# Optimization experiments

Hardware: AMD Instinct MI355X
Metric: run time of the kernel (lower is better)

Reference implementation:

```python
import jax, jax.numpy as jnp
import numpy as np

NUM_HEADS = 16
EPS = 1e-5
BLOCK = 16  # score_mod: q_idx // 16 == kv_idx % 16


def _ln(x, eps=EPS):
    # LayerNorm, elementwise_affine=False
    m = jnp.mean(x, axis=-1, keepdims=True)
    v = jnp.mean((x - m) ** 2, axis=-1, keepdims=True)
    return (x - m) * jax.lax.rsqrt(v + eps)


def setup_inputs() -> dict:
    key = jax.random.key(0)
    ks = jax.random.split(key, 5)
    N, D = 2048, 2048
    w = 0.02
    return {
        "x": jax.random.normal(ks[0], (N, D), jnp.float32),
        "Wq": jax.random.normal(ks[1], (D, D), jnp.float32) * w,
        "Wk": jax.random.normal(ks[2], (D, D), jnp.float32) * w,
        "Wv": jax.random.normal(ks[3], (D, D), jnp.float32) * w,
        "Wo": jax.random.normal(ks[4], (D, D), jnp.float32) * w,
    }


def reference(x, Wq, Wk, Wv, Wo):
    N, D = x.shape
    H = NUM_HEADS
    DH = D // H
    x_in = x
    xn = _ln(x)
    # per-head q/k layernorm, cast to attention dtype (bfloat16)
    q = _ln((xn @ Wq).reshape(N, H, DH)).astype(jnp.bfloat16)
    k = _ln((xn @ Wk).reshape(N, H, DH)).astype(jnp.bfloat16)
    v = (xn @ Wv).reshape(N, H, DH)  # stays fp32 (original applies no cast to vs)
    scale = 1.0 / np.sqrt(DH)
    # dense scores then sparsity mask, as flex_attention with score_mod does
    scores = jnp.einsum("nhd,mhd->hnm", q, k, preferred_element_type=jnp.float32) * scale
    qi = jnp.arange(N)
    mask = (qi[:, None] // BLOCK) == (qi[None, :] % BLOCK)  # [N, N]
    s = jnp.where(mask[None, :, :], scores, -jnp.inf)
    # safe softmax: rows with no allowed keys (q_idx >= 256) produce zeros
    mx = jnp.max(s, axis=-1, keepdims=True)
    e = jnp.exp(s - jnp.where(jnp.isfinite(mx), mx, 0.0))
    denom = jnp.sum(e, axis=-1, keepdims=True)
    attn = e / jnp.maximum(denom, 1e-30)
    o = jnp.einsum("hnm,mhd->nhd", attn, v)  # [N, H, DH]
    out = o.reshape(N, D) @ Wo
    return out + x_in
```

## Files before the change

kernel.cpp:

```cpp
#include <hip/hip_runtime.h>

typedef unsigned short u16;
typedef __attribute__((ext_vector_type(8))) short short8;
typedef __attribute__((ext_vector_type(4))) float f32x4;

#define D 2048
#define EPS 1e-5f

__device__ __forceinline__ u16 f2bf(float f) {
  unsigned u = __float_as_uint(f);
  u += 0x7fffu + ((u >> 16) & 1u);
  return (u16)(u >> 16);
}

__device__ __forceinline__ void async16(const void* g, void* l) {
  __builtin_amdgcn_global_load_lds(
      (const __attribute__((address_space(1))) void*)g,
      (__attribute__((address_space(3))) void*)l, 16, 0, 0);
}

__global__ __launch_bounds__(256) void prep(const float* __restrict__ x,
                                            const float* __restrict__ Wq,
                                            const float* __restrict__ Wk,
                                            const float* __restrict__ Wv,
                                            const float* __restrict__ Wo,
                                            u16* __restrict__ xn,
                                            float* __restrict__ out,
                                            u16* __restrict__ WqT, u16* __restrict__ WkT,
                                            u16* __restrict__ WvT, u16* __restrict__ WoT) {
  int bid = blockIdx.x;
  int t = threadIdx.x;
  if (bid < 2048) {
    const float* xr = x + (size_t)bid * D;
    float4 v[2];
    float s = 0.f, sq = 0.f;
#pragma unroll
    for (int i = 0; i < 2; i++) {
      v[i] = *(const float4*)(xr + i * 1024 + t * 4);
      s += v[i].x + v[i].y + v[i].z + v[i].w;
      sq += v[i].x * v[i].x + v[i].y * v[i].y + v[i].z * v[i].z + v[i].w * v[i].w;
    }
#pragma unroll
    for (int m = 32; m >= 1; m >>= 1) { s += __shfl_xor(s, m); sq += __shfl_xor(sq, m); }
    __shared__ float ps[4], pq[4];
    int w = t >> 6, lane = t & 63;
    if (lane == 0) { ps[w] = s; pq[w] = sq; }
    __syncthreads();
    s = ps[0] + ps[1] + ps[2] + ps[3];
    sq = pq[0] + pq[1] + pq[2] + pq[3];
    float mean = s * (1.f / D);
    float var = sq * (1.f / D) - mean * mean;
    float rs = rsqrtf(var + EPS);
    float* outr = out + (size_t)bid * D;
    u16* xnr = xn + (size_t)bid * D;
#pragma unroll
    for (int i = 0; i < 2; i++) {
      *(float4*)(outr + i * 1024 + t * 4) = v[i];
      ushort4 o;
      o.x = f2bf((v[i].x - mean) * rs);
      o.y = f2bf((v[i].y - mean) * rs);
      o.z = f2bf((v[i].z - mean) * rs);
      o.w = f2bf((v[i].w - mean) * rs);
      *(ushort4*)(xnr + i * 1024 + t * 4) = o;
    }
  } else {
    int tb = bid - 2048;
    int wsel = tb >> 10;
    int tt = tb & 1023;
    const float* src; u16* dst;
    switch (wsel) {
      case 0: src = Wq; dst = WqT; break;
      case 1: src = Wk; dst = WkT; break;
      case 2: src = Wv; dst = WvT; break;
      default: src = Wo; dst = WoT; break;
    }
    int i0 = (tt >> 5) * 64, j0 = (tt & 31) * 64;
    __shared__ u16 tile[64 * 66];
#pragma unroll
    for (int r = 0; r < 4; r++) {
      int idx = r * 256 + t;
      int row = idx >> 4, c4 = idx & 15;
      float4 v = *(const float4*)(src + (size_t)(i0 + row) * D + j0 + c4 * 4);
      tile[row * 66 + c4 * 4 + 0] = f2bf(v.x);
      tile[row * 66 + c4 * 4 + 1] = f2bf(v.y);
      tile[row * 66 + c4 * 4 + 2] = f2bf(v.z);
      tile[row * 66 + c4 * 4 + 3] = f2bf(v.w);
    }
    __syncthreads();
#pragma unroll
    for (int r = 0; r < 4; r++) {
      int idx = r * 256 + t;
      int row = idx >> 4, c4 = idx & 15;
      ushort4 o;
      o.x = tile[(c4 * 4 + 0) * 66 + row];
      o.y = tile[(c4 * 4 + 1) * 66 + row];
      o.z = tile[(c4 * 4 + 2) * 66 + row];
      o.w = tile[(c4 * 4 + 3) * 66 + row];
      *(ushort4*)(dst + (size_t)(j0 + row) * D + i0 + c4 * 4) = o;
    }
  }
}

__device__ __forceinline__ void gemm_tile(const u16* __restrict__ A,
                                          const u16* __restrict__ Bt,
                                          int m0, int n0,
                                          int kbeg, int kend,
                                          u16* As, u16* Bs, f32x4 acc[4][4]) {
  int tid = threadIdx.x, wid = tid >> 6, lane = tid & 63;
  int q4 = lane >> 4, m16 = lane & 15;
  int wm = wid >> 1, wn = wid & 1;
  for (int kb = kbeg; kb < kend; kb += 64) {
#pragma unroll
    for (int p = 0; p < 4; p++) {
      int idx = p * 256 + tid;
      int r = idx >> 3, sl = idx & 7;
      int gc = sl ^ (r & 7);
      async16(A + (size_t)(m0 + r) * D + kb + gc * 8, As + (size_t)idx * 8);
      async16(Bt + (size_t)(n0 + r) * D + kb + gc * 8, Bs + (size_t)idx * 8);
    }
    __syncthreads();
#pragma unroll
    for (int ks = 0; ks < 2; ks++) {
      short8 af[4], bf[4];
      int c = ks * 4 + q4;
#pragma unroll
      for (int i = 0; i < 4; i++) {
        int ra = wm * 64 + i * 16 + m16;
        af[i] = *(const short8*)(As + ra * 64 + (c ^ (ra & 7)) * 8);
        int rb = wn * 64 + i * 16 + m16;
        bf[i] = *(const short8*)(Bs + rb * 64 + (c ^ (rb & 7)) * 8);
      }
#pragma unroll
      for (int i = 0; i < 4; i++)
#pragma unroll
        for (int j = 0; j < 4; j++)
          acc[i][j] = __builtin_amdgcn_mfma_f32_16x16x32_bf16(af[i], bf[j], acc[i][j], 0, 0, 0);
    }
    __syncthreads();
  }
}

__global__ __launch_bounds__(256, 4) void gemm_mega(const u16* __restrict__ xn,
                                                    const u16* __restrict__ WkT,
                                                    const u16* __restrict__ WqT,
                                                    const u16* __restrict__ WvT,
                                                    u16* __restrict__ K3,
                                                    u16* __restrict__ Q3,
                                                    u16* __restrict__ V3) {
  __shared__ u16 smem[64 * 64 + 128 * 64];
  u16* As = smem;
  u16* Bs = smem + 64 * 64;
  int bid = blockIdx.x;
  int sel = (bid < 512) ? 0 : (bid < 1024) ? 2 : 1;
  int z = (sel == 0) ? bid : (sel == 2) ? bid - 512 : bid - 1024;
  int m0 = (z >> 4) * 64, n0 = (z & 15) * 128;
  const u16* A = (sel == 2) ? WvT : xn;
  const u16* Bt = (sel == 0) ? WkT : (sel == 1) ? WqT : xn;
  bool permB = (sel == 2);

  int tid = threadIdx.x, wid = tid >> 6, lane = tid & 63;
  int q4 = lane >> 4, m16 = lane & 15;
  int wm = wid >> 1, wn = wid & 1;

  f32x4 acc[2][4];
#pragma unroll
  for (int i = 0; i < 2; i++)
#pragma unroll
    for (int j = 0; j < 4; j++)
#pragma unroll
      for (int r = 0; r < 4; r++) acc[i][j][r] = 0.f;

  for (int kb = 0; kb < D; kb += 64) {
#pragma unroll
    for (int p = 0; p < 2; p++) {
      int idx = p * 256 + tid;
      int r = idx >> 3, sl = idx & 7;
      int gc = sl ^ (r & 7);
      async16(A + (size_t)(m0 + r) * D + kb + gc * 8, As + (size_t)idx * 8);
    }
#pragma unroll
    for (int p = 0; p < 4; p++) {
      int idx = p * 256 + tid;
      int r = idx >> 3, sl = idx & 7;
      int gc = sl ^ (r & 7);
      int rb = n0 + r;
      int gr = permB ? ((rb & 127) * 16 + (rb >> 7)) : rb;
      async16(Bt + (size_t)gr * D + kb + gc * 8, Bs + (size_t)idx * 8);
    }
    __syncthreads();
#pragma unroll
    for (int ks = 0; ks < 2; ks++) {
      short8 af[2], bf[4];
      int c = ks * 4 + q4;
#pragma unroll
      for (int i = 0; i < 2; i++) {
        int ra = wm * 32 + i * 16 + m16;
        af[i] = *(const short8*)(As + ra * 64 + (c ^ (ra & 7)) * 8);
      }
#pragma unroll
      for (int j = 0; j < 4; j++) {
        int rb = wn * 64 + j * 16 + m16;
        bf[j] = *(const short8*)(Bs + rb * 64 + (c ^ (rb & 7)) * 8);
      }
#pragma unroll
      for (int i = 0; i < 2; i++)
#pragma unroll
        for (int j = 0; j < 4; j++)
          acc[i][j] = __builtin_amdgcn_mfma_f32_16x16x32_bf16(af[i], bf[j], acc[i][j], 0, 0, 0);
    }
    __syncthreads();
  }

  if (sel == 2) {
    int h = m0 >> 7, b = n0 >> 7;
#pragma unroll
    for (int i = 0; i < 2; i++)
#pragma unroll
      for (int j = 0; j < 4; j++)
#pragma unroll
        for (int r = 0; r < 4; r++) {
          int dhl = (m0 & 127) + wm * 32 + i * 16 + q4 * 4 + r;
          int key = wn * 64 + j * 16 + m16;
          V3[((size_t)(h * 16 + b) * 128 + dhl) * 128 + key] = f2bf(acc[i][j][r]);
        }
  } else {
    float* redS = (float*)smem;
    float* redQ = redS + 128;
    __syncthreads();
#pragma unroll
    for (int i = 0; i < 2; i++) {
      float ps[4], pq[4];
#pragma unroll
      for (int r = 0; r < 4; r++) {
        float s = 0.f, q = 0.f;
#pragma unroll
        for (int j = 0; j < 4; j++) { float a = acc[i][j][r]; s += a; q += a * a; }
#pragma unroll
        for (int msk = 1; msk < 16; msk <<= 1) {
          s += __shfl_xor(s, msk);
          q += __shfl_xor(q, msk);
        }
        ps[r] = s; pq[r] = q;
      }
      if (m16 == 0) {
#pragma unroll
        for (int r = 0; r < 4; r++) {
          int row = wm * 32 + i * 16 + q4 * 4 + r;
          redS[row * 2 + wn] = ps[r];
          redQ[row * 2 + wn] = pq[r];
        }
      }
    }
    __syncthreads();
    int h = n0 >> 7;
#pragma unroll
    for (int i = 0; i < 2; i++)
#pragma unroll
      for (int r = 0; r < 4; r++) {
        int row = wm * 32 + i * 16 + q4 * 4 + r;
        float S = redS[row * 2] + redS[row * 2 + 1];
        float Qs = redQ[row * 2] + redQ[row * 2 + 1];
        float mean = S * (1.f / 128.f);
        float var = Qs * (1.f / 128.f) - mean * mean;
        float rstd = rsqrtf(var + EPS);
        int tok = m0 + row;
#pragma unroll
        for (int j = 0; j < 4; j++) {
          int dhl = wn * 64 + j * 16 + m16;
          u16 val = f2bf((acc[i][j][r] - mean) * rstd);
          if (sel == 0)
            K3[(((size_t)(h * 16 + (tok & 15))) * 128 + (tok >> 4)) * 128 + dhl] = val;
          else
            Q3[((size_t)h * 256 + tok) * 128 + dhl] = val;
        }
      }
  }
}

__global__ __launch_bounds__(128) void attn(const u16* __restrict__ Q3,
                                            const u16* __restrict__ K3,
                                            const u16* __restrict__ V3,
                                            u16* __restrict__ Ob) {
  int bh = blockIdx.x;
  int b = bh & 15, h = bh >> 4;
  int tid = threadIdx.x, w = tid >> 6, lane = tid & 63;
  int q4 = lane >> 4, m16 = lane & 15;
  __shared__ float redmx[2][16];
  __shared__ float redsm[2][16];
  __shared__ float invd[16];
  __shared__ u16 P[16][136];
  const float scale = 0.08838834764831845f;
  const u16* Ktile = K3 + (size_t)(h * 16 + b) * 128 * 128;
  const u16* Vtile = V3 + (size_t)(h * 16 + b) * 128 * 128;

  short8 af[4];
#pragma unroll
  for (int dc = 0; dc < 4; dc++)
    af[dc] = *(const short8*)(Q3 + ((size_t)h * 256 + b * 16 + m16) * 128 + dc * 32 + q4 * 8);
  f32x4 s[4];
#pragma unroll
  for (int kt = 0; kt < 4; kt++)
#pragma unroll
    for (int r = 0; r < 4; r++) s[kt][r] = 0.f;
#pragma unroll
  for (int kt = 0; kt < 4; kt++) {
    int key = w * 64 + kt * 16 + m16;
#pragma unroll
    for (int dc = 0; dc < 4; dc++) {
      short8 bf = *(const short8*)(Ktile + (size_t)key * 128 + dc * 32 + q4 * 8);
      s[kt] = __builtin_amdgcn_mfma_f32_16x16x32_bf16(af[dc], bf, s[kt], 0, 0, 0);
    }
  }
  float mx[4];
#pragma unroll
  for (int r = 0; r < 4; r++) {
    mx[r] = fmaxf(fmaxf(s[0][r], s[1][r]), fmaxf(s[2][r], s[3][r]));
#pragma unroll
    for (int msk = 1; msk < 16; msk <<= 1) mx[r] = fmaxf(mx[r], __shfl_xor(mx[r], msk));
  }
  if (m16 == 0) {
#pragma unroll
    for (int r = 0; r < 4; r++) redmx[w][q4 * 4 + r] = mx[r];
  }
  __syncthreads();
#pragma unroll
  for (int r = 0; r < 4; r++) {
    float M = fmaxf(redmx[0][q4 * 4 + r], redmx[1][q4 * 4 + r]);
    float acc = 0.f;
#pragma unroll
    for (int kt = 0; kt < 4; kt++) {
      float e = __expf((s[kt][r] - M) * scale);
      s[kt][r] = e;
      acc += e;
    }
#pragma unroll
    for (int msk = 1; msk < 16; msk <<= 1) acc += __shfl_xor(acc, msk);
    if (m16 == 0) redsm[w][q4 * 4 + r] = acc;
  }
#pragma unroll
  for (int kt = 0; kt < 4; kt++)
#pragma unroll
    for (int r = 0; r < 4; r++)
      P[q4 * 4 + r][w * 64 + kt * 16 + m16] = f2bf(s[kt][r]);
  __syncthreads();
  if (tid < 16) invd[tid] = 1.0f / (redsm[0][tid] + redsm[1][tid]);
  __syncthreads();

  short8 pf[4];
#pragma unroll
  for (int kc = 0; kc < 4; kc++)
    pf[kc] = *(const short8*)(&P[m16][kc * 32 + q4 * 8]);
  f32x4 o[4];
#pragma unroll
  for (int dt = 0; dt < 4; dt++)
#pragma unroll
    for (int r = 0; r < 4; r++) o[dt][r] = 0.f;
#pragma unroll
  for (int dt = 0; dt < 4; dt++) {
    int dhl = (w * 4 + dt) * 16 + m16;
#pragma unroll
    for (int kc = 0; kc < 4; kc++) {
      short8 vf = *(const short8*)(Vtile + (size_t)dhl * 128 + kc * 32 + q4 * 8);
      o[dt] = __builtin_amdgcn_mfma_f32_16x16x32_bf16(pf[kc], vf, o[dt], 0, 0, 0);
    }
  }
#pragma unroll
  for (int dt = 0; dt < 4; dt++)
#pragma unroll
    for (int r = 0; r < 4; r++) {
      int row = q4 * 4 + r;
      float val = o[dt][r] * invd[row];
      Ob[(size_t)(b * 16 + row) * D + h * 128 + (w * 4 + dt) * 16 + m16] = f2bf(val);
    }
}

__global__ __launch_bounds__(256, 3) void gemm_wo(const u16* __restrict__ Ob,
                                                  const u16* __restrict__ WoT,
                                                  float* __restrict__ Wpart) {
  __shared__ u16 smem[2 * 128 * 64];
  u16* As = smem;
  u16* Bs = smem + 8192;
  int m0 = blockIdx.x * 128, n0 = blockIdx.y * 128;
  int z = blockIdx.z;
  int k0 = z * 256;
  f32x4 acc[4][4];
#pragma unroll
  for (int i = 0; i < 4; i++)
#pragma unroll
    for (int j = 0; j < 4; j++)
#pragma unroll
      for (int r = 0; r < 4; r++) acc[i][j][r] = 0.f;
  gemm_tile(Ob, WoT, m0, n0, k0, k0 + 256, As, Bs, acc);
  float* C = Wpart + (size_t)z * 256 * D;
  int tid = threadIdx.x, wid = tid >> 6, lane = tid & 63;
  int q4 = lane >> 4, m16 = lane & 15;
  int wm = wid >> 1, wn = wid & 1;
#pragma unroll
  for (int i = 0; i < 4; i++)
#pragma unroll
    for (int j = 0; j < 4; j++)
#pragma unroll
      for (int r = 0; r < 4; r++) {
        int row = m0 + wm * 64 + i * 16 + q4 * 4 + r;
        int col = n0 + wn * 64 + j * 16 + m16;
        C[(size_t)row * D + col] = acc[i][j][r];
      }
}

__global__ __launch_bounds__(256) void reduce_wo(const float* __restrict__ Wpart,
                                                 float* __restrict__ out) {
  int i = (blockIdx.x * 256 + threadIdx.x) * 4;
  float4 s = *(const float4*)(out + i);
#pragma unroll
  for (int z = 0; z < 8; z++) {
    float4 p = *(const float4*)(Wpart + (size_t)z * 256 * D + i);
    s.x += p.x; s.y += p.y; s.z += p.z; s.w += p.w;
  }
  *(float4*)(out + i) = s;
}

extern "C" void kernel_launch(void* const* d_in, const int* in_sizes, int n_in,
                              void* d_out, int out_size, void* d_ws, size_t ws_size,
                              hipStream_t stream) {
  const float* x  = (const float*)d_in[0];
  const float* Wq = (const float*)d_in[1];
  const float* Wk = (const float*)d_in[2];
  const float* Wv = (const float*)d_in[3];
  const float* Wo = (const float*)d_in[4];
  float* out = (float*)d_out;
  char* w = (char*)d_ws;
  const size_t MB = 1u << 20;
  u16*   xn    = (u16*)(w);
  u16*   WqT   = (u16*)(w + 8 * MB);
  u16*   WkT   = (u16*)(w + 16 * MB);
  u16*   WvT   = (u16*)(w + 24 * MB);
  u16*   WoT   = (u16*)(w + 32 * MB);
  u16*   K3    = (u16*)(w + 40 * MB);
  u16*   V3    = (u16*)(w + 48 * MB);
  u16*   Q3    = (u16*)(w + 56 * MB);
  u16*   Obf   = (u16*)(w + 57 * MB);
  float* Wpart = (float*)(w + 58 * MB);

  prep<<<dim3(6144), dim3(256), 0, stream>>>(x, Wq, Wk, Wv, Wo, xn, out, WqT, WkT, WvT, WoT);
  gemm_mega<<<dim3(1088), dim3(256), 0, stream>>>(xn, WkT, WqT, WvT, K3, Q3, V3);
  attn<<<dim3(256), dim3(128), 0, stream>>>(Q3, K3, V3, Obf);
  gemm_wo<<<dim3(2, 16, 8), dim3(256), 0, stream>>>(Obf, WoT, Wpart);
  reduce_wo<<<dim3(512), dim3(256), 0, stream>>>(Wpart, out);
}
```

Before: 200.2 us.

## Split prep into layernorm and wide-tile weight transpose, widen attention to four waves

The combined prep kernel is split into a row layernorm kernel and a separate weight transpose-and-convert kernel. The transpose now uses 128x128 tiles and writes 16-byte vectors instead of 8-byte ones, to improve global store coalescing. The attention kernel goes from two to four waves per block, each handling 32 keys and 32 output columns, to spread the small per-block work over more lanes. The trade-off is one extra kernel launch and a larger LDS tile in the transpose kernel.

```diff
diff --git a/kernel.cpp b/kernel.cpp
--- a/kernel.cpp
+++ b/kernel.cpp
@@ -19,85 +19,81 @@
       (__attribute__((address_space(3))) void*)l, 16, 0, 0);
 }
 
-__global__ __launch_bounds__(256) void prep(const float* __restrict__ x,
-                                            const float* __restrict__ Wq,
-                                            const float* __restrict__ Wk,
-                                            const float* __restrict__ Wv,
-                                            const float* __restrict__ Wo,
-                                            u16* __restrict__ xn,
-                                            float* __restrict__ out,
-                                            u16* __restrict__ WqT, u16* __restrict__ WkT,
-                                            u16* __restrict__ WvT, u16* __restrict__ WoT) {
+__global__ __launch_bounds__(256) void ln_rows(const float* __restrict__ x,
+                                               u16* __restrict__ xn,
+                                               float* __restrict__ out) {
   int bid = blockIdx.x;
   int t = threadIdx.x;
-  if (bid < 2048) {
-    const float* xr = x + (size_t)bid * D;
-    float4 v[2];
-    float s = 0.f, sq = 0.f;
-#pragma unroll
-    for (int i = 0; i < 2; i++) {
-      v[i] = *(const float4*)(xr + i * 1024 + t * 4);
-      s += v[i].x + v[i].y + v[i].z + v[i].w;
-      sq += v[i].x * v[i].x + v[i].y * v[i].y + v[i].z * v[i].z + v[i].w * v[i].w;
-    }
-#pragma unroll
-    for (int m = 32; m >= 1; m >>= 1) { s += __shfl_xor(s, m); sq += __shfl_xor(sq, m); }
-    __shared__ float ps[4], pq[4];
-    int w = t >> 6, lane = t & 63;
-    if (lane == 0) { ps[w] = s; pq[w] = sq; }
-    __syncthreads();
-    s = ps[0] + ps[1] + ps[2] + ps[3];
-    sq = pq[0] + pq[1] + pq[2] + pq[3];
-    float mean = s * (1.f / D);
-    float var = sq * (1.f / D) - mean * mean;
-    float rs = rsqrtf(var + EPS);
-    float* outr = out + (size_t)bid * D;
-    u16* xnr = xn + (size_t)bid * D;
-#pragma unroll
-    for (int i = 0; i < 2; i++) {
-      *(float4*)(outr + i * 1024 + t * 4) = v[i];
-      ushort4 o;
-      o.x = f2bf((v[i].x - mean) * rs);
-      o.y = f2bf((v[i].y - mean) * rs);
-      o.z = f2bf((v[i].z - mean) * rs);
-      o.w = f2bf((v[i].w - mean) * rs);
-      *(ushort4*)(xnr + i * 1024 + t * 4) = o;
-    }
-  } else {
-    int tb = bid - 2048;
-    int wsel = tb >> 10;
-    int tt = tb & 1023;
-    const float* src; u16* dst;
-    switch (wsel) {
-      case 0: src = Wq; dst = WqT; break;
-      case 1: src = Wk; dst = WkT; break;
-      case 2: src = Wv; dst = WvT; break;
-      default: src = Wo; dst = WoT; break;
-    }
-    int i0 = (tt >> 5) * 64, j0 = (tt & 31) * 64;
-    __shared__ u16 tile[64 * 66];
-#pragma unroll
-    for (int r = 0; r < 4; r++) {
-      int idx = r * 256 + t;
-      int row = idx >> 4, c4 = idx & 15;
-      float4 v = *(const float4*)(src + (size_t)(i0 + row) * D + j0 + c4 * 4);
-      tile[row * 66 + c4 * 4 + 0] = f2bf(v.x);
-      tile[row * 66 + c4 * 4 + 1] = f2bf(v.y);
-      tile[row * 66 + c4 * 4 + 2] = f2bf(v.z);
-      tile[row * 66 + c4 * 4 + 3] = f2bf(v.w);
-    }
-    __syncthreads();
-#pragma unroll
-    for (int r = 0; r < 4; r++) {
-      int idx = r * 256 + t;
-      int row = idx >> 4, c4 = idx & 15;
-      ushort4 o;
-      o.x = tile[(c4 * 4 + 0) * 66 + row];
-      o.y = tile[(c4 * 4 + 1) * 66 + row];
-      o.z = tile[(c4 * 4 + 2) * 66 + row];
-      o.w = tile[(c4 * 4 + 3) * 66 + row];
-      *(ushort4*)(dst + (size_t)(j0 + row) * D + i0 + c4 * 4) = o;
-    }
+  const float* xr = x + (size_t)bid * D;
+  float4 v[2];
+  float s = 0.f, sq = 0.f;
+#pragma unroll
+  for (int i = 0; i < 2; i++) {
+    v[i] = *(const float4*)(xr + i * 1024 + t * 4);
+    s += v[i].x + v[i].y + v[i].z + v[i].w;
+    sq += v[i].x * v[i].x + v[i].y * v[i].y + v[i].z * v[i].z + v[i].w * v[i].w;
+  }
+#pragma unroll
+  for (int m = 32; m >= 1; m >>= 1) { s += __shfl_xor(s, m); sq += __shfl_xor(sq, m); }
+  __shared__ float ps[4], pq[4];
+  int w = t >> 6, lane = t & 63;
+  if (lane == 0) { ps[w] = s; pq[w] = sq; }
+  __syncthreads();
+  s = ps[0] + ps[1] + ps[2] + ps[3];
+  sq = pq[0] + pq[1] + pq[2] + pq[3];
+  float mean = s * (1.f / D);
+  float var = sq * (1.f / D) - mean * mean;
+  float rs = rsqrtf(var + EPS);
+  float* outr = out + (size_t)bid * D;
+  u16* xnr = xn + (size_t)bid * D;
+#pragma unroll
+  for (int i = 0; i < 2; i++) {
+    *(float4*)(outr + i * 1024 + t * 4) = v[i];
+    ushort4 o;
+    o.x = f2bf((v[i].x - mean) * rs);
+    o.y = f2bf((v[i].y - mean) * rs);
+    o.z = f2bf((v[i].z - mean) * rs);
+    o.w = f2bf((v[i].w - mean) * rs);
+    *(ushort4*)(xnr + i * 1024 + t * 4) = o;
+  }
+}
+
+__global__ __launch_bounds__(256) void transpose_cvt(
+    const float* __restrict__ Wq, const float* __restrict__ Wk,
+    const float* __restrict__ Wv, const float* __restrict__ Wo,
+    u16* __restrict__ WqT, u16* __restrict__ WkT,
+    u16* __restrict__ WvT, u16* __restrict__ WoT) {
+  int bid = blockIdx.x;
+  int wsel = bid >> 8;
+  int tt = bid & 255;
+  const float* src; u16* dst;
+  switch (wsel) {
+    case 0: src = Wq; dst = WqT; break;
+    case 1: src = Wk; dst = WkT; break;
+    case 2: src = Wv; dst = WvT; break;
+    default: src = Wo; dst = WoT; break;
+  }
+  int k0 = (tt >> 4) * 128, n0 = (tt & 15) * 128;
+  __shared__ u16 tile[128 * 136];
+  int t = threadIdx.x;
+#pragma unroll
+  for (int i = 0; i < 16; i++) {
+    int idx = i * 256 + t;
+    int k = idx >> 5, c4 = idx & 31;
+    float4 v = *(const float4*)(src + (size_t)(k0 + k) * D + n0 + c4 * 4);
+    int n = c4 * 4;
+    tile[(n + 0) * 136 + k] = f2bf(v.x);
+    tile[(n + 1) * 136 + k] = f2bf(v.y);
+    tile[(n + 2) * 136 + k] = f2bf(v.z);
+    tile[(n + 3) * 136 + k] = f2bf(v.w);
+  }
+  __syncthreads();
+#pragma unroll
+  for (int i = 0; i < 8; i++) {
+    int idx = i * 256 + t;
+    int n = idx >> 4, kc = idx & 15;
+    short8 v = *(const short8*)(tile + n * 136 + kc * 8);
+    *(short8*)(dst + (size_t)(n0 + n) * D + k0 + kc * 8) = v;
   }
 }
 
@@ -277,7 +273,7 @@
   }
 }
 
-__global__ __launch_bounds__(128) void attn(const u16* __restrict__ Q3,
+__global__ __launch_bounds__(256) void attn(const u16* __restrict__ Q3,
                                             const u16* __restrict__ K3,
                                             const u16* __restrict__ V3,
                                             u16* __restrict__ Ob) {
@@ -285,8 +281,8 @@
   int b = bh & 15, h = bh >> 4;
   int tid = threadIdx.x, w = tid >> 6, lane = tid & 63;
   int q4 = lane >> 4, m16 = lane & 15;
-  __shared__ float redmx[2][16];
-  __shared__ float redsm[2][16];
+  __shared__ float redmx[4][16];
+  __shared__ float redsm[4][16];
   __shared__ float invd[16];
   __shared__ u16 P[16][136];
   const float scale = 0.08838834764831845f;
@@ -297,14 +293,14 @@
 #pragma unroll
   for (int dc = 0; dc < 4; dc++)
     af[dc] = *(const short8*)(Q3 + ((size_t)h * 256 + b * 16 + m16) * 128 + dc * 32 + q4 * 8);
-  f32x4 s[4];
-#pragma unroll
-  for (int kt = 0; kt < 4; kt++)
+  f32x4 s[2];
+#pragma unroll
+  for (int kt = 0; kt < 2; kt++)
 #pragma unroll
     for (int r = 0; r < 4; r++) s[kt][r] = 0.f;
 #pragma unroll
-  for (int kt = 0; kt < 4; kt++) {
-    int key = w * 64 + kt * 16 + m16;
+  for (int kt = 0; kt < 2; kt++) {
+    int key = w * 32 + kt * 16 + m16;
 #pragma unroll
     for (int dc = 0; dc < 4; dc++) {
       short8 bf = *(const short8*)(Ktile + (size_t)key * 128 + dc * 32 + q4 * 8);
@@ -314,7 +310,7 @@
   float mx[4];
 #pragma unroll
   for (int r = 0; r < 4; r++) {
-    mx[r] = fmaxf(fmaxf(s[0][r], s[1][r]), fmaxf(s[2][r], s[3][r]));
+    mx[r] = fmaxf(s[0][r], s[1][r]);
 #pragma unroll
     for (int msk = 1; msk < 16; msk <<= 1) mx[r] = fmaxf(mx[r], __shfl_xor(mx[r], msk));
   }
@@ -325,39 +321,42 @@
   __syncthreads();
 #pragma unroll
   for (int r = 0; r < 4; r++) {
-    float M = fmaxf(redmx[0][q4 * 4 + r], redmx[1][q4 * 4 + r]);
+    int row = q4 * 4 + r;
+    float M = fmaxf(fmaxf(redmx[0][row], redmx[1][row]),
+                    fmaxf(redmx[2][row], redmx[3][row]));
     float acc = 0.f;
 #pragma unroll
-    for (int kt = 0; kt < 4; kt++) {
+    for (int kt = 0; kt < 2; kt++) {
       float e = __expf((s[kt][r] - M) * scale);
       s[kt][r] = e;
       acc += e;
     }
 #pragma unroll
     for (int msk = 1; msk < 16; msk <<= 1) acc += __shfl_xor(acc, msk);
-    if (m16 == 0) redsm[w][q4 * 4 + r] = acc;
-  }
-#pragma unroll
-  for (int kt = 0; kt < 4; kt++)
+    if (m16 == 0) redsm[w][row] = acc;
+  }
+#pragma unroll
+  for (int kt = 0; kt < 2; kt++)
 #pragma unroll
     for (int r = 0; r < 4; r++)
-      P[q4 * 4 + r][w * 64 + kt * 16 + m16] = f2bf(s[kt][r]);
+      P[q4 * 4 + r][w * 32 + kt * 16 + m16] = f2bf(s[kt][r]);
   __syncthreads();
-  if (tid < 16) invd[tid] = 1.0f / (redsm[0][tid] + redsm[1][tid]);
+  if (tid < 16)
+    invd[tid] = 1.0f / (redsm[0][tid] + redsm[1][tid] + redsm[2][tid] + redsm[3][tid]);
   __syncthreads();
 
   short8 pf[4];
 #pragma unroll
   for (int kc = 0; kc < 4; kc++)
     pf[kc] = *(const short8*)(&P[m16][kc * 32 + q4 * 8]);
-  f32x4 o[4];
-#pragma unroll
-  for (int dt = 0; dt < 4; dt++)
+  f32x4 o[2];
+#pragma unroll
+  for (int dt = 0; dt < 2; dt++)
 #pragma unroll
     for (int r = 0; r < 4; r++) o[dt][r] = 0.f;
 #pragma unroll
-  for (int dt = 0; dt < 4; dt++) {
-    int dhl = (w * 4 + dt) * 16 + m16;
+  for (int dt = 0; dt < 2; dt++) {
+    int dhl = w * 32 + dt * 16 + m16;
 #pragma unroll
     for (int kc = 0; kc < 4; kc++) {
       short8 vf = *(const short8*)(Vtile + (size_t)dhl * 128 + kc * 32 + q4 * 8);
@@ -365,12 +364,12 @@
     }
   }
 #pragma unroll
-  for (int dt = 0; dt < 4; dt++)
+  for (int dt = 0; dt < 2; dt++)
 #pragma unroll
     for (int r = 0; r < 4; r++) {
       int row = q4 * 4 + r;
       float val = o[dt][r] * invd[row];
-      Ob[(size_t)(b * 16 + row) * D + h * 128 + (w * 4 + dt) * 16 + m16] = f2bf(val);
+      Ob[(size_t)(b * 16 + row) * D + h * 128 + w * 32 + dt * 16 + m16] = f2bf(val);
     }
 }
 
@@ -441,9 +440,10 @@
   u16*   Obf   = (u16*)(w + 57 * MB);
   float* Wpart = (float*)(w + 58 * MB);
 
-  prep<<<dim3(6144), dim3(256), 0, stream>>>(x, Wq, Wk, Wv, Wo, xn, out, WqT, WkT, WvT, WoT);
+  ln_rows<<<dim3(2048), dim3(256), 0, stream>>>(x, xn, out);
+  transpose_cvt<<<dim3(1024), dim3(256), 0, stream>>>(Wq, Wk, Wv, Wo, WqT, WkT, WvT, WoT);
   gemm_mega<<<dim3(1088), dim3(256), 0, stream>>>(xn, WkT, WqT, WvT, K3, Q3, V3);
-  attn<<<dim3(256), dim3(128), 0, stream>>>(Q3, K3, V3, Obf);
+  attn<<<dim3(256), dim3(256), 0, stream>>>(Q3, K3, V3, Obf);
   gemm_wo<<<dim3(2, 16, 8), dim3(256), 0, stream>>>(Obf, WoT, Wpart);
   reduce_wo<<<dim3(512), dim3(256), 0, stream>>>(Wpart, out);
 }
```

Measured after the change: 197.7 us. Within noise of the previous version (-1.2%).
